# Performance work log

Hardware: AMD Instinct MI355X
Metric: run time of the kernel (lower is better)

Reference implementation:

```python
import jax, jax.numpy as jnp
import numpy as np
from jax import lax

H = 1024   # hidden_size
I = 1024   # input_size
O = 2 * H  # output_size (must equal 2H for decoder_input feedback)
T = 8192   # encoder sequence length
L = 64     # MAX_LENGTH


def _uniform(key, shape, scale):
    return jax.random.uniform(key, shape, jnp.float32, -scale, scale)


def setup_inputs() -> dict:
    key = jax.random.key(0)
    ks = jax.random.split(key, 18)
    s = 1.0 / float(np.sqrt(H))
    return {
        "x": jax.random.normal(ks[0], (T, 1, I), jnp.float32),
        "h0": jnp.zeros((2, 1, H), jnp.float32),
        # encoder GRU, forward direction
        "enc_Wih_f": _uniform(ks[1], (3 * H, I), s),
        "enc_Whh_f": _uniform(ks[2], (3 * H, H), s),
        "enc_bih_f": _uniform(ks[3], (3 * H,), s),
        "enc_bhh_f": _uniform(ks[4], (3 * H,), s),
        # encoder GRU, backward direction
        "enc_Wih_b": _uniform(ks[5], (3 * H, I), s),
        "enc_Whh_b": _uniform(ks[6], (3 * H, H), s),
        "enc_bih_b": _uniform(ks[7], (3 * H,), s),
        "enc_bhh_b": _uniform(ks[8], (3 * H,), s),
        # decoder GRU (input = cat(decoder_input[2H], context[2H]) = 4H)
        "dec_Wih": _uniform(ks[9], (3 * H, 4 * H), s),
        "dec_Whh": _uniform(ks[10], (3 * H, H), s),
        "dec_bih": _uniform(ks[11], (3 * H,), s),
        "dec_bhh": _uniform(ks[12], (3 * H,), s),
        # attention: Linear(3H, 1) applied to cat(dec_hidden[H], enc_out[2H])
        "W_att": _uniform(ks[13], (1, 3 * H), 1.0 / float(np.sqrt(3 * H))),
        "b_att": _uniform(ks[14], (1,), 1.0 / float(np.sqrt(3 * H))),
        # output projection Linear(H, O)
        "W_out": _uniform(ks[15], (O, H), s),
        "b_out": _uniform(ks[16], (O,), s),
        "max_length": L,
    }


def gru_cell(x, h, Wih, Whh, bih, bhh):
    # PyTorch GRU cell math; x [B,in], h [B,H]
    gi = x @ Wih.T + bih
    gh = h @ Whh.T + bhh
    ir, iz, inn = jnp.split(gi, 3, axis=-1)
    hr, hz, hn = jnp.split(gh, 3, axis=-1)
    r = jax.nn.sigmoid(ir + hr)
    z = jax.nn.sigmoid(iz + hz)
    n = jnp.tanh(inn + r * hn)
    return (1.0 - z) * n + z * h


def run_gru(xs, h0, Wih, Whh, bih, bhh):
    def step(h, x):  # x [1,in]
        h = gru_cell(x, h, Wih, Whh, bih, bhh)
        return h, h
    hT, outs = lax.scan(step, h0, xs)
    return outs, hT  # outs [T,1,H]


def reference(x, h0, enc_Wih_f, enc_Whh_f, enc_bih_f, enc_bhh_f,
              enc_Wih_b, enc_Whh_b, enc_bih_b, enc_bhh_b,
              dec_Wih, dec_Whh, dec_bih, dec_bhh,
              W_att, b_att, W_out, b_out, max_length):
    # bidirectional encoder
    out_f, h_f = run_gru(x, h0[0], enc_Wih_f, enc_Whh_f, enc_bih_f, enc_bhh_f)
    out_b_rev, h_b = run_gru(x[::-1], h0[1], enc_Wih_b, enc_Whh_b, enc_bih_b, enc_bhh_b)
    enc = jnp.concatenate([out_f, out_b_rev[::-1]], axis=-1)  # [T,1,2H]
    enc2 = enc[:, 0, :]                                        # [T,2H]

    # split attention weight per cat order: (decoder_hidden[H], enc_out[2H])
    W_att_h = W_att[:, :H]   # [1,H]
    W_att_e = W_att[:, H:]   # [1,2H]
    enc_scores = enc2 @ W_att_e.T  # [T,1], precomputed (batched replaces python loop)

    dec_in0 = jnp.zeros((1, 2 * H), x.dtype)
    h_dec0 = h_b  # encoder_hidden[-1] is the backward-direction final state

    def step(carry, _):
        dec_in, h = carry
        scores = (enc_scores + (h @ W_att_h.T)[0] + b_att)[:, 0]  # [T]
        attn = jax.nn.softmax(scores)
        context = attn @ enc2                                     # [2H]
        xin = jnp.concatenate([dec_in, context[None, :]], axis=-1)  # [1,4H]
        h_new = gru_cell(xin, h, dec_Wih, dec_Whh, dec_bih, dec_bhh)
        out = jax.nn.log_softmax(h_new @ W_out.T + b_out, axis=1)  # [1,O]
        return (lax.stop_gradient(out), h_new), out  # .detach() feedback

    _, outs = lax.scan(step, (dec_in0, h_dec0), None, length=max_length)
    return outs  # [L,1,O] stacked log-probs
```

## Files before the change

kernel.cpp:

```cpp
#include <hip/hip_runtime.h>
#include <hip/hip_bf16.h>

typedef __hip_bfloat16 bf16_t;
typedef unsigned long long u64;
struct alignas(8) bh4 { bf16_t v[4]; };
__device__ __forceinline__ float bf2f(bf16_t v) { return __bfloat162float(v); }

static constexpr size_t OFF_ENC2   = 25165824;
static constexpr size_t OFF_SCORES = OFF_ENC2 + 16777216;
static constexpr size_t OFF_CTX    = OFF_SCORES + 8192;
static constexpr size_t OFF_GICTX  = OFF_CTX + 2048;
static constexpr size_t OFF_PUB    = OFF_GICTX + 4096;

static constexpr unsigned TAG_BAD = 0x7FFFFFFFu;

__device__ __forceinline__ u64 pub_load(const u64* p) {
  return __hip_atomic_load(p, __ATOMIC_RELAXED, __HIP_MEMORY_SCOPE_AGENT);
}
__device__ __forceinline__ void pub_store(u64* p, u64 v) {
  __hip_atomic_store(p, v, __ATOMIC_RELAXED, __HIP_MEMORY_SCOPE_AGENT);
}
__device__ __forceinline__ u64 pack(unsigned tag, float f) {
  union { float f; unsigned u; } c; c.f = f;
  return ((u64)tag << 32) | c.u;
}
__device__ __forceinline__ float unpack(u64 w) {
  union { unsigned u; float f; } c; c.u = (unsigned)w;
  return c.f;
}

__global__ __launch_bounds__(1024) void k_init(const float* __restrict__ h0,
                                               u64* pub) {
  int i = blockIdx.x * 1024 + threadIdx.x;
  if (i < 1024)       pub[i] = pack(0u, h0[i]);
  else if (i < 2048)  pub[i] = pack(TAG_BAD, 0.f);
  else if (i < 3072)  pub[i] = pack(0u, h0[1024 + (i - 2048)]);
  else if (i < 10240) pub[i] = pack(TAG_BAD, 0.f);
}

__global__ __launch_bounds__(256) void k_gemm_gi(
    const float* __restrict__ X, const float* __restrict__ Wf,
    const float* __restrict__ Wb, const float* __restrict__ bf,
    const float* __restrict__ bb, bf16_t* __restrict__ GI) {
  __shared__ __align__(16) float As[16][68];
  __shared__ __align__(16) float Bs[16][68];
  const int m0 = blockIdx.x * 64;
  const int n0 = blockIdx.y * 64;
  const int tid = threadIdx.x;
  const int tx = tid & 15, ty = tid >> 4;
  const int lm = tid >> 2, lk = (tid & 3) * 4;
  const float* Wsel = (n0 < 3072) ? Wf : Wb;
  const float* bsel = (n0 < 3072) ? bf : bb;
  const int nadj = (n0 < 3072) ? n0 : (n0 - 3072);
  float acc[4][4];
#pragma unroll
  for (int i = 0; i < 4; ++i)
#pragma unroll
    for (int j = 0; j < 4; ++j) acc[i][j] = 0.f;
  for (int k0 = 0; k0 < 1024; k0 += 16) {
    float4 av = *(const float4*)(X + (size_t)(m0 + lm) * 1024 + k0 + lk);
    float4 bv = *(const float4*)(Wsel + (size_t)(nadj + lm) * 1024 + k0 + lk);
    __syncthreads();
    As[lk + 0][lm] = av.x; As[lk + 1][lm] = av.y; As[lk + 2][lm] = av.z; As[lk + 3][lm] = av.w;
    Bs[lk + 0][lm] = bv.x; Bs[lk + 1][lm] = bv.y; Bs[lk + 2][lm] = bv.z; Bs[lk + 3][lm] = bv.w;
    __syncthreads();
#pragma unroll
    for (int kk = 0; kk < 16; ++kk) {
      float4 a = *(const float4*)&As[kk][ty * 4];
      float4 b = *(const float4*)&Bs[kk][tx * 4];
      acc[0][0] += a.x * b.x; acc[0][1] += a.x * b.y; acc[0][2] += a.x * b.z; acc[0][3] += a.x * b.w;
      acc[1][0] += a.y * b.x; acc[1][1] += a.y * b.y; acc[1][2] += a.y * b.z; acc[1][3] += a.y * b.w;
      acc[2][0] += a.z * b.x; acc[2][1] += a.z * b.y; acc[2][2] += a.z * b.z; acc[2][3] += a.z * b.w;
      acc[3][0] += a.w * b.x; acc[3][1] += a.w * b.y; acc[3][2] += a.w * b.z; acc[3][3] += a.w * b.w;
    }
  }
  float b0 = bsel[nadj + tx * 4 + 0], b1 = bsel[nadj + tx * 4 + 1];
  float b2 = bsel[nadj + tx * 4 + 2], b3 = bsel[nadj + tx * 4 + 3];
#pragma unroll
  for (int i = 0; i < 4; ++i) {
    bh4 o;
    o.v[0] = __float2bfloat16(acc[i][0] + b0);
    o.v[1] = __float2bfloat16(acc[i][1] + b1);
    o.v[2] = __float2bfloat16(acc[i][2] + b2);
    o.v[3] = __float2bfloat16(acc[i][3] + b3);
    *(bh4*)(GI + (size_t)(m0 + ty * 4 + i) * 6144 + n0 + tx * 4) = o;
  }
}

__global__ __launch_bounds__(1024, 1) void k_recurrence(
    const bf16_t* __restrict__ GI, const float* __restrict__ Whh_f,
    const float* __restrict__ Whh_b, const float* __restrict__ bhh_f,
    const float* __restrict__ bhh_b, float* __restrict__ enc2,
    u64* pub_f, u64* pub_b) {
  __shared__ __align__(16) float w[24][1024];
  __shared__ __align__(16) float hsh[1024];
  __shared__ float rowsum[24];
  __shared__ float bsh[24];
  __shared__ float gish[24];
  const int blk = blockIdx.x;
  const int dir = blk >> 7;
  const int bb = blk & 127;
  const int j0 = bb * 8;
  const int tid = threadIdx.x;
  const int wv = tid >> 6, lane = tid & 63;
  const float* Whh = dir ? Whh_b : Whh_f;
  const float* bhh = dir ? bhh_b : bhh_f;
  u64* pub = dir ? pub_b : pub_f;

  for (int i = tid; i < 24 * 256; i += 1024) {
    int r = i >> 8, c4 = i & 255;
    int g = r >> 3, jj = r & 7;
    *(float4*)&w[r][c4 * 4] =
        *(const float4*)(Whh + (size_t)(g * 1024 + j0 + jj) * 1024 + c4 * 4);
  }
  if (tid < 24) {
    int g = tid >> 3, jj = tid & 7;
    bsh[tid] = bhh[g * 1024 + j0 + jj];
  }
  float gpre = 0.f;
  size_t gcol = 0;
  if (tid < 24) {
    int g = tid >> 3, jj = tid & 7;
    gcol = (size_t)(dir ? 3072 : 0) + g * 1024 + j0 + jj;
    gpre = bf2f(GI[(size_t)(dir ? 8191 : 0) * 6144 + gcol]);
  }
  __syncthreads();

  for (int t = 0; t < 8192; ++t) {
    {
      u64* src = pub + (size_t)(t & 1) * 1024 + tid;
      u64 wd = pub_load(src);
      while ((unsigned)(wd >> 32) != (unsigned)t) {
        __builtin_amdgcn_s_sleep(1);
        wd = pub_load(src);
      }
      hsh[tid] = unpack(wd);
    }
    __syncthreads();
    if (tid < 24) {
      gish[tid] = gpre;
      if (t < 8191) {
        size_t row = dir ? (size_t)(8190 - t) : (size_t)(t + 1);
        gpre = bf2f(GI[row * 6144 + gcol]);
      }
    }
    float a0 = 0.f, a1 = 0.f;
    {
      const float4* hp = (const float4*)hsh;
      const float4* w0 = (const float4*)&w[wv][0];
#pragma unroll
      for (int q = 0; q < 4; ++q) {
        int idx = lane + 64 * q;
        float4 hv = hp[idx], x0 = w0[idx];
        a0 += hv.x * x0.x + hv.y * x0.y + hv.z * x0.z + hv.w * x0.w;
      }
      if (wv < 8) {
        const float4* w1 = (const float4*)&w[16 + wv][0];
#pragma unroll
        for (int q = 0; q < 4; ++q) {
          int idx = lane + 64 * q;
          float4 hv = hp[idx], x1 = w1[idx];
          a1 += hv.x * x1.x + hv.y * x1.y + hv.z * x1.z + hv.w * x1.w;
        }
      }
    }
#pragma unroll
    for (int off = 32; off; off >>= 1) {
      a0 += __shfl_xor(a0, off);
      a1 += __shfl_xor(a1, off);
    }
    if (lane == 0) {
      rowsum[wv] = a0;
      if (wv < 8) rowsum[16 + wv] = a1;
    }
    __syncthreads();
    if (tid < 8) {
      int jj = tid, j = j0 + jj;
      float hr = rowsum[jj] + bsh[jj];
      float hz = rowsum[8 + jj] + bsh[8 + jj];
      float hn = rowsum[16 + jj] + bsh[16 + jj];
      float ir = gish[jj], iz = gish[8 + jj], inn = gish[16 + jj];
      float rr = 1.f / (1.f + expf(-(ir + hr)));
      float zz = 1.f / (1.f + expf(-(iz + hz)));
      float nn = tanhf(inn + rr * hn);
      float hnew = (1.f - zz) * nn + zz * hsh[j];
      pub_store(pub + (size_t)((t + 1) & 1) * 1024 + j, pack((unsigned)(t + 1), hnew));
      size_t trow = dir ? (size_t)(8191 - t) : (size_t)t;
      enc2[trow * 2048 + dir * 1024 + j] = hnew;
    }
  }
}

__global__ __launch_bounds__(256) void k_scores(const float* __restrict__ enc2,
                                                const float* __restrict__ Watt,
                                                const float* __restrict__ batt,
                                                float* __restrict__ scores) {
  int wv = threadIdx.x >> 6, lane = threadIdx.x & 63;
  int t = blockIdx.x * 4 + wv;
  const float* We = Watt + 1024;
  float a = 0.f;
#pragma unroll
  for (int k = 0; k < 8; ++k) {
    float4 e = *(const float4*)(enc2 + (size_t)t * 2048 + lane * 4 + k * 256);
    float4 ww = *(const float4*)(We + lane * 4 + k * 256);
    a += e.x * ww.x + e.y * ww.y + e.z * ww.z + e.w * ww.w;
  }
#pragma unroll
  for (int off = 32; off; off >>= 1) a += __shfl_xor(a, off);
  if (lane == 0) scores[t] = a + batt[0];
}

__global__ __launch_bounds__(256) void k_softmax(float* __restrict__ s) {
  __shared__ float red[8];
  int tid = threadIdx.x, wv = tid >> 6, lane = tid & 63;
  float m = -1e30f;
  for (int i = tid; i < 8192; i += 256) m = fmaxf(m, s[i]);
#pragma unroll
  for (int off = 32; off; off >>= 1) m = fmaxf(m, __shfl_xor(m, off));
  if (lane == 0) red[wv] = m;
  __syncthreads();
  m = fmaxf(fmaxf(red[0], red[1]), fmaxf(red[2], red[3]));
  float sum = 0.f;
  for (int i = tid; i < 8192; i += 256) sum += expf(s[i] - m);
#pragma unroll
  for (int off = 32; off; off >>= 1) sum += __shfl_xor(sum, off);
  if (lane == 0) red[4 + wv] = sum;
  __syncthreads();
  sum = red[4] + red[5] + red[6] + red[7];
  float inv = 1.0f / sum;
  for (int i = tid; i < 8192; i += 256) s[i] = expf(s[i] - m) * inv;
}

__global__ __launch_bounds__(256) void k_context(const float* __restrict__ attn,
                                                 const float* __restrict__ enc2,
                                                 float* __restrict__ ctx) {
  int k = blockIdx.x * 256 + threadIdx.x;
  float a0 = 0.f, a1 = 0.f, a2 = 0.f, a3 = 0.f;
  for (int t = 0; t < 8192; t += 4) {
    a0 += attn[t] * enc2[(size_t)t * 2048 + k];
    a1 += attn[t + 1] * enc2[(size_t)(t + 1) * 2048 + k];
    a2 += attn[t + 2] * enc2[(size_t)(t + 2) * 2048 + k];
    a3 += attn[t + 3] * enc2[(size_t)(t + 3) * 2048 + k];
  }
  ctx[k] = (a0 + a1) + (a2 + a3);
}

__global__ __launch_bounds__(256) void k_gictx(const float* __restrict__ dWih,
                                               const float* __restrict__ dbih,
                                               const float* __restrict__ ctx,
                                               float* __restrict__ gictx) {
  int wv = threadIdx.x >> 6, lane = threadIdx.x & 63;
  int i = blockIdx.x * 4 + wv;
  float a = 0.f;
#pragma unroll
  for (int k = 0; k < 8; ++k) {
    float4 ww = *(const float4*)(dWih + (size_t)i * 4096 + 2048 + lane * 4 + k * 256);
    float4 c = *(const float4*)(ctx + lane * 4 + k * 256);
    a += ww.x * c.x + ww.y * c.y + ww.z * c.z + ww.w * c.w;
  }
#pragma unroll
  for (int off = 32; off; off >>= 1) a += __shfl_xor(a, off);
  if (lane == 0) gictx[i] = a + dbih[i];
}

__global__ void k_decinit(const u64* __restrict__ pub_b, u64* hpub) {
  int i = threadIdx.x;
  hpub[i] = pack(0u, unpack(pub_b[i]));
}

__global__ __launch_bounds__(1024, 1) void k_decoder(
    const float* __restrict__ gictx, const float* __restrict__ dWih,
    const float* __restrict__ dWhh, const float* __restrict__ dbhh,
    const float* __restrict__ Wout, const float* __restrict__ bout,
    u64* hpub, u64* lpub, float* __restrict__ out) {
  __shared__ __align__(16) float hsh[1024];
  __shared__ __align__(16) float lsh[2048];
  __shared__ __align__(16) float dsh[2048];
  __shared__ float rsA[24], rsB[24];
  __shared__ float red[32];
  __shared__ float gctx[24], bsh[24], bo[16];
  const int bb = blockIdx.x;
  const int j0 = bb * 8, o0 = bb * 16;
  const int tid = threadIdx.x, wv = tid >> 6, lane = tid & 63;
  if (tid < 24) {
    int g = tid >> 3, jj = tid & 7;
    gctx[tid] = gictx[g * 1024 + j0 + jj];
    bsh[tid] = dbhh[g * 1024 + j0 + jj];
  }
  if (tid < 16) bo[tid] = bout[o0 + tid];
  __syncthreads();

  for (int s = 0; s < 64; ++s) {
    {
      u64* hp = hpub + (size_t)(s & 1) * 1024 + tid;
      u64 wd = pub_load(hp);
      while ((unsigned)(wd >> 32) != (unsigned)s) {
        __builtin_amdgcn_s_sleep(1);
        wd = pub_load(hp);
      }
      hsh[tid] = unpack(wd);
    }
    if (s > 0) {
      u64* lp = lpub + (size_t)(s & 1) * 2048;
#pragma unroll
      for (int q = 0; q < 2; ++q) {
        int i = tid + q * 1024;
        u64 wd = pub_load(lp + i);
        while ((unsigned)(wd >> 32) != (unsigned)s) {
          __builtin_amdgcn_s_sleep(1);
          wd = pub_load(lp + i);
        }
        lsh[i] = unpack(wd);
      }
    }
    __syncthreads();
    if (s > 0) {
      float m = fmaxf(lsh[tid], lsh[tid + 1024]);
#pragma unroll
      for (int off = 32; off; off >>= 1) m = fmaxf(m, __shfl_xor(m, off));
      if (lane == 0) red[wv] = m;
      __syncthreads();
      m = -1e30f;
      for (int i = 0; i < 16; ++i) m = fmaxf(m, red[i]);
      float e = expf(lsh[tid] - m) + expf(lsh[tid + 1024] - m);
#pragma unroll
      for (int off = 32; off; off >>= 1) e += __shfl_xor(e, off);
      if (lane == 0) red[16 + wv] = e;
      __syncthreads();
      float se = 0.f;
      for (int i = 0; i < 16; ++i) se += red[16 + i];
      float c = m + logf(se);
      dsh[tid] = lsh[tid] - c;
      dsh[tid + 1024] = lsh[tid + 1024] - c;
    } else {
      dsh[tid] = 0.f;
      dsh[tid + 1024] = 0.f;
    }
    __syncthreads();
    if (s > 0 && tid < 16) out[(size_t)(s - 1) * 2048 + o0 + tid] = dsh[o0 + tid];
    float aA0 = 0.f, aB0 = 0.f, aA1 = 0.f, aB1 = 0.f;
    {
      int g = wv >> 3, jj = wv & 7;
      const float4* rowI = (const float4*)(dWih + (size_t)(g * 1024 + j0 + jj) * 4096);
      const float4* rowH = (const float4*)(dWhh + (size_t)(g * 1024 + j0 + jj) * 1024);
      const float4* dp = (const float4*)dsh;
      const float4* hp = (const float4*)hsh;
#pragma unroll
      for (int q = 0; q < 8; ++q) {
        int idx = lane + 64 * q;
        float4 d = dp[idx], wi = rowI[idx];
        aA0 += d.x * wi.x + d.y * wi.y + d.z * wi.z + d.w * wi.w;
      }
#pragma unroll
      for (int q = 0; q < 4; ++q) {
        int idx = lane + 64 * q;
        float4 h = hp[idx], wh = rowH[idx];
        aB0 += h.x * wh.x + h.y * wh.y + h.z * wh.z + h.w * wh.w;
      }
      if (wv < 8) {
        const float4* rowI2 = (const float4*)(dWih + (size_t)(2 * 1024 + j0 + wv) * 4096);
        const float4* rowH2 = (const float4*)(dWhh + (size_t)(2 * 1024 + j0 + wv) * 1024);
#pragma unroll
        for (int q = 0; q < 8; ++q) {
          int idx = lane + 64 * q;
          float4 d = dp[idx], wi = rowI2[idx];
          aA1 += d.x * wi.x + d.y * wi.y + d.z * wi.z + d.w * wi.w;
        }
#pragma unroll
        for (int q = 0; q < 4; ++q) {
          int idx = lane + 64 * q;
          float4 h = hp[idx], wh = rowH2[idx];
          aB1 += h.x * wh.x + h.y * wh.y + h.z * wh.z + h.w * wh.w;
        }
      }
    }
#pragma unroll
    for (int off = 32; off; off >>= 1) {
      aA0 += __shfl_xor(aA0, off); aB0 += __shfl_xor(aB0, off);
      aA1 += __shfl_xor(aA1, off); aB1 += __shfl_xor(aB1, off);
    }
    if (lane == 0) {
      rsA[wv] = aA0; rsB[wv] = aB0;
      if (wv < 8) { rsA[16 + wv] = aA1; rsB[16 + wv] = aB1; }
    }
    __syncthreads();
    if (tid < 8) {
      int jj = tid, j = j0 + jj;
      float ir = gctx[jj] + rsA[jj];
      float iz = gctx[8 + jj] + rsA[8 + jj];
      float inn = gctx[16 + jj] + rsA[16 + jj];
      float hr = rsB[jj] + bsh[jj];
      float hz = rsB[8 + jj] + bsh[8 + jj];
      float hn = rsB[16 + jj] + bsh[16 + jj];
      float rr = 1.f / (1.f + expf(-(ir + hr)));
      float zz = 1.f / (1.f + expf(-(iz + hz)));
      float nn = tanhf(inn + rr * hn);
      float hnew = (1.f - zz) * nn + zz * hsh[j];
      pub_store(hpub + (size_t)((s + 1) & 1) * 1024 + j, pack((unsigned)(s + 1), hnew));
    }
    __syncthreads();
    {
      u64* hp = hpub + (size_t)((s + 1) & 1) * 1024 + tid;
      u64 wd = pub_load(hp);
      while ((unsigned)(wd >> 32) != (unsigned)(s + 1)) {
        __builtin_amdgcn_s_sleep(1);
        wd = pub_load(hp);
      }
      hsh[tid] = unpack(wd);
    }
    __syncthreads();
    {
      int o = o0 + wv;
      const float4* rowO = (const float4*)(Wout + (size_t)o * 1024);
      const float4* hp = (const float4*)hsh;
      float l = 0.f;
#pragma unroll
      for (int q = 0; q < 4; ++q) {
        int idx = lane + 64 * q;
        float4 h = hp[idx], wo = rowO[idx];
        l += h.x * wo.x + h.y * wo.y + h.z * wo.z + h.w * wo.w;
      }
#pragma unroll
      for (int off = 32; off; off >>= 1) l += __shfl_xor(l, off);
      if (lane == 0)
        pub_store(lpub + (size_t)((s + 1) & 1) * 2048 + o, pack((unsigned)(s + 1), l + bo[wv]));
    }
    __syncthreads();
  }
  {
    u64* lp = lpub + 0;
#pragma unroll
    for (int q = 0; q < 2; ++q) {
      int i = tid + q * 1024;
      u64 wd = pub_load(lp + i);
      while ((unsigned)(wd >> 32) != 64u) {
        __builtin_amdgcn_s_sleep(1);
        wd = pub_load(lp + i);
      }
      lsh[i] = unpack(wd);
    }
  }
  __syncthreads();
  float m = fmaxf(lsh[tid], lsh[tid + 1024]);
#pragma unroll
  for (int off = 32; off; off >>= 1) m = fmaxf(m, __shfl_xor(m, off));
  if (lane == 0) red[wv] = m;
  __syncthreads();
  m = -1e30f;
  for (int i = 0; i < 16; ++i) m = fmaxf(m, red[i]);
  float e = expf(lsh[tid] - m) + expf(lsh[tid + 1024] - m);
#pragma unroll
  for (int off = 32; off; off >>= 1) e += __shfl_xor(e, off);
  if (lane == 0) red[16 + wv] = e;
  __syncthreads();
  float se = 0.f;
  for (int i = 0; i < 16; ++i) se += red[16 + i];
  float c = m + logf(se);
  if (tid < 16) out[(size_t)63 * 2048 + o0 + tid] = lsh[o0 + tid] - c;
}

extern "C" void kernel_launch(void* const* d_in, const int* in_sizes, int n_in,
                              void* d_out, int out_size, void* d_ws, size_t ws_size,
                              hipStream_t stream) {
  (void)in_sizes; (void)n_in; (void)out_size; (void)ws_size;
  const float* x      = (const float*)d_in[0];
  const float* h0     = (const float*)d_in[1];
  const float* eWih_f = (const float*)d_in[2];
  const float* eWhh_f = (const float*)d_in[3];
  const float* ebih_f = (const float*)d_in[4];
  const float* ebhh_f = (const float*)d_in[5];
  const float* eWih_b = (const float*)d_in[6];
  const float* eWhh_b = (const float*)d_in[7];
  const float* ebih_b = (const float*)d_in[8];
  const float* ebhh_b = (const float*)d_in[9];
  const float* dWih   = (const float*)d_in[10];
  const float* dWhh   = (const float*)d_in[11];
  const float* dbih   = (const float*)d_in[12];
  const float* dbhh   = (const float*)d_in[13];
  const float* Watt   = (const float*)d_in[14];
  const float* batt   = (const float*)d_in[15];
  const float* Wout   = (const float*)d_in[16];
  const float* bout   = (const float*)d_in[17];

  float* ws = (float*)d_ws;
  bf16_t* GI    = (bf16_t*)d_ws;
  float* enc2   = ws + OFF_ENC2;
  float* scores = ws + OFF_SCORES;
  float* ctx    = ws + OFF_CTX;
  float* gictx  = ws + OFF_GICTX;
  u64* pub      = (u64*)(ws + OFF_PUB);
  u64* pub_f = pub;
  u64* pub_b = pub + 2048;
  u64* hpub  = pub + 4096;
  u64* lpub  = pub + 6144;
  float* out = (float*)d_out;

  k_init<<<10, 1024, 0, stream>>>(h0, pub);
  k_gemm_gi<<<dim3(128, 96), 256, 0, stream>>>(x, eWih_f, eWih_b, ebih_f, ebih_b, GI);
  k_recurrence<<<256, 1024, 0, stream>>>(GI, eWhh_f, eWhh_b, ebhh_f, ebhh_b, enc2, pub_f, pub_b);
  k_scores<<<2048, 256, 0, stream>>>(enc2, Watt, batt, scores);
  k_softmax<<<1, 256, 0, stream>>>(scores);
  k_context<<<8, 256, 0, stream>>>(scores, enc2, ctx);
  k_gictx<<<768, 256, 0, stream>>>(dWih, dbih, ctx, gictx);
  k_decinit<<<1, 1024, 0, stream>>>(pub_b, hpub);
  k_decoder<<<128, 1024, 0, stream>>>(gictx, dWih, dWhh, dbhh, Wout, bout, hpub, lpub, out);
}
```

Before: 23.02 ms.

## Keep recurrent weights in registers and drop the second barrier per step

The encoder recurrence kernel now keeps each hidden unit's three Whh rows in registers of one wavefront, instead of spreading 24 rows across 16 wavefronts in shared memory. Each wavefront reduces its own r/z/n dot products and applies the gate math directly, which removes the rowsum exchange and one __syncthreads per timestep. The h buffer is double-buffered so one barrier per step stays safe. The gates also switch to fast __expf-based sigmoid/tanh. Only 8 of 16 wavefronts do compute, and register pressure rises.

```diff
diff --git a/kernel.cpp b/kernel.cpp
--- a/kernel.cpp
+++ b/kernel.cpp
@@ -27,6 +27,13 @@
 __device__ __forceinline__ float unpack(u64 w) {
   union { unsigned u; float f; } c; c.u = (unsigned)w;
   return c.f;
+}
+__device__ __forceinline__ float fsigmoid(float x) {
+  return 1.f / (1.f + __expf(-x));
+}
+__device__ __forceinline__ float ftanh(float x) {
+  float e2 = __expf(2.f * x);
+  return 1.f - 2.f / (e2 + 1.f);
 }
 
 __global__ __launch_bounds__(1024) void k_init(const float* __restrict__ h0,
@@ -92,11 +99,9 @@
     const float* __restrict__ Whh_b, const float* __restrict__ bhh_f,
     const float* __restrict__ bhh_b, float* __restrict__ enc2,
     u64* pub_f, u64* pub_b) {
-  __shared__ __align__(16) float w[24][1024];
-  __shared__ __align__(16) float hsh[1024];
-  __shared__ float rowsum[24];
-  __shared__ float bsh[24];
-  __shared__ float gish[24];
+  __shared__ __align__(16) float smem[25600];
+  float* hsh0 = smem;
+  float* hsh1 = smem + 1024;
   const int blk = blockIdx.x;
   const int dir = blk >> 7;
   const int bb = blk & 127;
@@ -107,26 +112,31 @@
   const float* bhh = dir ? bhh_b : bhh_f;
   u64* pub = dir ? pub_b : pub_f;
 
-  for (int i = tid; i < 24 * 256; i += 1024) {
-    int r = i >> 8, c4 = i & 255;
-    int g = r >> 3, jj = r & 7;
-    *(float4*)&w[r][c4 * 4] =
-        *(const float4*)(Whh + (size_t)(g * 1024 + j0 + jj) * 1024 + c4 * 4);
-  }
-  if (tid < 24) {
-    int g = tid >> 3, jj = tid & 7;
-    bsh[tid] = bhh[g * 1024 + j0 + jj];
-  }
-  float gpre = 0.f;
-  size_t gcol = 0;
-  if (tid < 24) {
-    int g = tid >> 3, jj = tid & 7;
-    gcol = (size_t)(dir ? 3072 : 0) + g * 1024 + j0 + jj;
-    gpre = bf2f(GI[(size_t)(dir ? 8191 : 0) * 6144 + gcol]);
-  }
-  __syncthreads();
+  float4 wr0[4], wr1[4], wr2[4];
+  float br = 0.f, bz = 0.f, bn = 0.f;
+  float gir = 0.f, giz = 0.f, gin = 0.f;
+  size_t gbase = 0;
+  if (wv < 8) {
+    int j = j0 + wv;
+    const float* r0p = Whh + (size_t)(0 * 1024 + j) * 1024;
+    const float* r1p = Whh + (size_t)(1 * 1024 + j) * 1024;
+    const float* r2p = Whh + (size_t)(2 * 1024 + j) * 1024;
+#pragma unroll
+    for (int q = 0; q < 4; ++q) {
+      wr0[q] = *(const float4*)(r0p + 4 * lane + 256 * q);
+      wr1[q] = *(const float4*)(r1p + 4 * lane + 256 * q);
+      wr2[q] = *(const float4*)(r2p + 4 * lane + 256 * q);
+    }
+    br = bhh[j]; bz = bhh[1024 + j]; bn = bhh[2048 + j];
+    gbase = (size_t)(dir ? 3072 : 0) + j;
+    size_t row0 = dir ? (size_t)8191 : (size_t)0;
+    gir = bf2f(GI[row0 * 6144 + gbase]);
+    giz = bf2f(GI[row0 * 6144 + gbase + 1024]);
+    gin = bf2f(GI[row0 * 6144 + gbase + 2048]);
+  }
 
   for (int t = 0; t < 8192; ++t) {
+    float* hcur = (t & 1) ? hsh1 : hsh0;
     {
       u64* src = pub + (size_t)(t & 1) * 1024 + tid;
       u64 wd = pub_load(src);
@@ -134,59 +144,42 @@
         __builtin_amdgcn_s_sleep(1);
         wd = pub_load(src);
       }
-      hsh[tid] = unpack(wd);
-    }
-    __syncthreads();
-    if (tid < 24) {
-      gish[tid] = gpre;
-      if (t < 8191) {
-        size_t row = dir ? (size_t)(8190 - t) : (size_t)(t + 1);
-        gpre = bf2f(GI[row * 6144 + gcol]);
-      }
-    }
-    float a0 = 0.f, a1 = 0.f;
-    {
-      const float4* hp = (const float4*)hsh;
-      const float4* w0 = (const float4*)&w[wv][0];
+      hcur[tid] = unpack(wd);
+    }
+    __syncthreads();
+    if (wv < 8) {
+      const float4* hp = (const float4*)hcur;
+      float ar = 0.f, az = 0.f, an = 0.f;
 #pragma unroll
       for (int q = 0; q < 4; ++q) {
-        int idx = lane + 64 * q;
-        float4 hv = hp[idx], x0 = w0[idx];
-        a0 += hv.x * x0.x + hv.y * x0.y + hv.z * x0.z + hv.w * x0.w;
-      }
-      if (wv < 8) {
-        const float4* w1 = (const float4*)&w[16 + wv][0];
-#pragma unroll
-        for (int q = 0; q < 4; ++q) {
-          int idx = lane + 64 * q;
-          float4 hv = hp[idx], x1 = w1[idx];
-          a1 += hv.x * x1.x + hv.y * x1.y + hv.z * x1.z + hv.w * x1.w;
+        float4 hv = hp[lane + 64 * q];
+        ar += hv.x * wr0[q].x + hv.y * wr0[q].y + hv.z * wr0[q].z + hv.w * wr0[q].w;
+        az += hv.x * wr1[q].x + hv.y * wr1[q].y + hv.z * wr1[q].z + hv.w * wr1[q].w;
+        an += hv.x * wr2[q].x + hv.y * wr2[q].y + hv.z * wr2[q].z + hv.w * wr2[q].w;
+      }
+#pragma unroll
+      for (int off = 32; off; off >>= 1) {
+        ar += __shfl_xor(ar, off);
+        az += __shfl_xor(az, off);
+        an += __shfl_xor(an, off);
+      }
+      if (lane == 0) {
+        int j = j0 + wv;
+        float rr = fsigmoid(gir + ar + br);
+        float zz = fsigmoid(giz + az + bz);
+        float nn = ftanh(gin + rr * (an + bn));
+        float hnew = (1.f - zz) * nn + zz * hcur[j];
+        pub_store(pub + (size_t)((t + 1) & 1) * 1024 + j,
+                  pack((unsigned)(t + 1), hnew));
+        size_t trow = dir ? (size_t)(8191 - t) : (size_t)t;
+        enc2[trow * 2048 + dir * 1024 + j] = hnew;
+        if (t < 8191) {
+          size_t row = dir ? (size_t)(8190 - t) : (size_t)(t + 1);
+          gir = bf2f(GI[row * 6144 + gbase]);
+          giz = bf2f(GI[row * 6144 + gbase + 1024]);
+          gin = bf2f(GI[row * 6144 + gbase + 2048]);
         }
       }
-    }
-#pragma unroll
-    for (int off = 32; off; off >>= 1) {
-      a0 += __shfl_xor(a0, off);
-      a1 += __shfl_xor(a1, off);
-    }
-    if (lane == 0) {
-      rowsum[wv] = a0;
-      if (wv < 8) rowsum[16 + wv] = a1;
-    }
-    __syncthreads();
-    if (tid < 8) {
-      int jj = tid, j = j0 + jj;
-      float hr = rowsum[jj] + bsh[jj];
-      float hz = rowsum[8 + jj] + bsh[8 + jj];
-      float hn = rowsum[16 + jj] + bsh[16 + jj];
-      float ir = gish[jj], iz = gish[8 + jj], inn = gish[16 + jj];
-      float rr = 1.f / (1.f + expf(-(ir + hr)));
-      float zz = 1.f / (1.f + expf(-(iz + hz)));
-      float nn = tanhf(inn + rr * hn);
-      float hnew = (1.f - zz) * nn + zz * hsh[j];
-      pub_store(pub + (size_t)((t + 1) & 1) * 1024 + j, pack((unsigned)(t + 1), hnew));
-      size_t trow = dir ? (size_t)(8191 - t) : (size_t)t;
-      enc2[trow * 2048 + dir * 1024 + j] = hnew;
     }
   }
 }
```

Result: slower. 34.23 ms (+48.7%).
